# Kernel tuning notes

Measured on AMD Instinct MI355X. Metric: run time of the kernel, lower is better.

The kernel has to match this reference:

```python
import jax, jax.numpy as jnp
import numpy as np

N = 100000   # nodes
E = 1200000  # edges
D = 64       # feature / hidden dim (heads=1)
L = 3        # num_layers
G = 64       # num graphs
SCALE = 1.0 / np.sqrt(D)


def setup_inputs() -> dict:
    key = jax.random.key(0)
    ks = jax.random.split(key, 12)
    inp = {
        "x": jax.random.normal(ks[0], (N, D), dtype=jnp.float32),
        "edge_index": jax.random.randint(ks[1], (2, E), 0, N, dtype=jnp.int64),
        "batch": jnp.sort(jax.random.randint(ks[2], (N,), 0, G, dtype=jnp.int64)),
        "Wq": jax.random.normal(ks[3], (L, D, D), dtype=jnp.float32) * 0.1,
        "bq": jax.random.normal(ks[4], (L, D), dtype=jnp.float32) * 0.1,
        "Wk": jax.random.normal(ks[5], (L, D, D), dtype=jnp.float32) * 0.1,
        "bk": jax.random.normal(ks[6], (L, D), dtype=jnp.float32) * 0.1,
        "Wv": jax.random.normal(ks[7], (L, D, D), dtype=jnp.float32) * 0.1,
        "bv": jax.random.normal(ks[8], (L, D), dtype=jnp.float32) * 0.1,
        "Ws": jax.random.normal(ks[9], (L, D, D), dtype=jnp.float32) * 0.1,
        "bs": jax.random.normal(ks[10], (L, D), dtype=jnp.float32) * 0.1,
    }
    return inp


def _transformer_conv(x, src, dst, Wq, bq, Wk, bk, Wv, bv, Ws, bs):
    # PyG TransformerConv, heads=1, concat=True, root_weight=True, beta=False
    q = x @ Wq + bq            # [N, D] query of target nodes
    k = x @ Wk + bk            # [N, D] key of source nodes
    v = x @ Wv + bv            # [N, D] value of source nodes
    logits = jnp.sum(q[dst] * k[src], axis=-1) * SCALE  # [E]
    # segment softmax over incoming edges of each target node
    m = jax.ops.segment_max(logits, dst, num_segments=N)        # [N]
    e = jnp.exp(logits - m[dst])                                 # [E]
    denom = jax.ops.segment_sum(e, dst, num_segments=N)         # [N]
    alpha = e / denom[dst]                                       # [E]
    agg = jax.ops.segment_sum(alpha[:, None] * v[src], dst, num_segments=N)  # [N, D]
    return agg + x @ Ws + bs   # root/skip connection


def reference(x, edge_index, batch, Wq, bq, Wk, bk, Wv, bv, Ws, bs):
    src, dst = edge_index[0], edge_index[1]
    for l in range(L):
        x = _transformer_conv(x, src, dst, Wq[l], bq[l], Wk[l], bk[l],
                              Wv[l], bv[l], Ws[l], bs[l])
        x = jax.nn.relu(x)
    # global_mean_pool
    sums = jax.ops.segment_sum(x, batch, num_segments=G)                  # [G, D]
    counts = jax.ops.segment_sum(jnp.ones((N,), x.dtype), batch, num_segments=G)
    graph_emb = sums / jnp.maximum(counts, 1.0)[:, None]
    return (x, graph_emb)
```

## Files before the change

### kernel.cpp

```cpp
#include <hip/hip_runtime.h>
#include <math.h>

#define DD 64
#define APAD 512

typedef _Float16 h2 __attribute__((ext_vector_type(2)));
typedef _Float16 h4 __attribute__((ext_vector_type(4)));
typedef _Float16 h8 __attribute__((ext_vector_type(8)));
typedef float f32x4 __attribute__((ext_vector_type(4)));

__global__ __launch_bounds__(256) void k_prep(
    const float* __restrict__ Wq, const float* __restrict__ Wk,
    const float* __restrict__ Wv, const float* __restrict__ Ws,
    _Float16* __restrict__ wf,
    const float* __restrict__ x, _Float16* __restrict__ xb,
    int wblocks, int total8)
{
  int tid = threadIdx.x;
  if ((int)blockIdx.x < wblocks) {
    int id = blockIdx.x * 4 + (tid >> 6);
    int lane = tid & 63;
    int layer = id >> 5;
    int c = (id >> 1) & 15;
    int s = id & 1;
    int col = c * 16 + (lane & 15);
    int mi = col >> 6;
    const float* W = (mi == 0 ? Wq : mi == 1 ? Wk : mi == 2 ? Wv : Ws)
                     + (size_t)layer * DD * DD;
    int colw = col & 63;
    _Float16* o = wf + ((((size_t)(layer * 16 + c)) * 2 + s) * 64 + lane) * 8;
    #pragma unroll
    for (int j = 0; j < 8; ++j) {
      int k = s * 32 + (lane >> 4) * 8 + j;
      o[j] = (_Float16)W[k * DD + colw];
    }
  } else {
    int i = (blockIdx.x - wblocks) * 256 + tid;
    if (i >= total8) return;
    float4 a = ((const float4*)x)[i * 2];
    float4 b = ((const float4*)x)[i * 2 + 1];
    h8 o;
    o[0] = (_Float16)a.x; o[1] = (_Float16)a.y; o[2] = (_Float16)a.z; o[3] = (_Float16)a.w;
    o[4] = (_Float16)b.x; o[5] = (_Float16)b.y; o[6] = (_Float16)b.z; o[7] = (_Float16)b.w;
    *(h8*)(xb + (size_t)i * 8) = o;
  }
}

#define LH_STRIDE 200
#define LS_STRIDE 72
#define WAVE_LDS  (16 * 400 + 16 * 144)

__global__ __launch_bounds__(256) void k_projM(
    const _Float16* __restrict__ xb, const _Float16* __restrict__ wf,
    const float* __restrict__ bq, const float* __restrict__ bk,
    const float* __restrict__ bv, const float* __restrict__ bs,
    _Float16* __restrict__ qh, _Float16* __restrict__ kvh,
    _Float16* __restrict__ sh, int n)
{
  __shared__ __align__(16) char lds[4 * WAVE_LDS];
  int wave = threadIdx.x >> 6;
  int lane = threadIdx.x & 63;
  int nbase = blockIdx.x * 64 + wave * 16;
  if (nbase >= n) return;

  char* wbase = lds + wave * WAVE_LDS;
  _Float16* lh = (_Float16*)wbase;
  _Float16* ls = (_Float16*)(wbase + 16 * 400);

  const int cl = lane & 15;
  const int rq = lane >> 4;

  int ar = min(nbase + cl, n - 1);
  h8 a0 = *(const h8*)(xb + (size_t)ar * DD + rq * 8);
  h8 a1 = *(const h8*)(xb + (size_t)ar * DD + 32 + rq * 8);

  #pragma unroll
  for (int c = 0; c < 16; ++c) {
    const float* bp = (c < 4) ? bq : (c < 8) ? bk : (c < 12) ? bv : bs;
    const int fb = c * 16 + rq * 4;
    float4 b4 = *(const float4*)(bp + (fb & 63));
    f32x4 acc; acc[0] = b4.x; acc[1] = b4.y; acc[2] = b4.z; acc[3] = b4.w;
    const _Float16* wp = wf + ((size_t)(c * 2) * 64 + lane) * 8;
    h8 w0 = *(const h8*)(wp);
    h8 w1 = *(const h8*)(wp + 64 * 8);
    acc = __builtin_amdgcn_mfma_f32_16x16x32_f16(w0, a0, acc, 0, 0, 0);
    acc = __builtin_amdgcn_mfma_f32_16x16x32_f16(w1, a1, acc, 0, 0, 0);

    h4 o; o[0] = (_Float16)acc[0]; o[1] = (_Float16)acc[1];
    o[2] = (_Float16)acc[2]; o[3] = (_Float16)acc[3];
    if (c < 12)
      *(h4*)(lh + cl * LH_STRIDE + fb) = o;
    else
      *(h4*)(ls + cl * LS_STRIDE + (fb - 192)) = o;
  }

  #pragma unroll
  for (int i = 0; i < 2; ++i) {
    int chunk = i * 64 + lane;
    int nd = chunk >> 3, co = chunk & 7;
    h8 v = *(const h8*)(lh + nd * LH_STRIDE + co * 8);
    if (nbase + nd < n)
      *(h8*)(qh + (size_t)(nbase + nd) * DD + co * 8) = v;
  }
  #pragma unroll
  for (int i = 0; i < 4; ++i) {
    int chunk = i * 64 + lane;
    int nd = chunk >> 4, co = chunk & 15;
    h8 v = *(const h8*)(lh + nd * LH_STRIDE + 64 + co * 8);
    if (nbase + nd < n)
      *(h8*)(kvh + (size_t)(nbase + nd) * 128 + co * 8) = v;
  }
  #pragma unroll
  for (int i = 0; i < 2; ++i) {
    int chunk = i * 64 + lane;
    int nd = chunk >> 3, co = chunk & 7;
    h8 v = *(const h8*)(ls + nd * LS_STRIDE + co * 8);
    if (nbase + nd < n)
      *(h8*)(sh + (size_t)(nbase + nd) * DD + co * 8) = v;
  }
}

__global__ __launch_bounds__(256) void k_hist(
    const int* __restrict__ dst, int* __restrict__ deg,
    unsigned short* __restrict__ pos, int ecnt)
{
  int e = (blockIdx.x * 256 + threadIdx.x) * 4;
  if (e + 3 < ecnt) {
    int4 d = *(const int4*)(dst + e);
    pos[e]     = (unsigned short)atomicAdd(deg + d.x, 1);
    pos[e + 1] = (unsigned short)atomicAdd(deg + d.y, 1);
    pos[e + 2] = (unsigned short)atomicAdd(deg + d.z, 1);
    pos[e + 3] = (unsigned short)atomicAdd(deg + d.w, 1);
  } else {
    for (; e < ecnt; ++e)
      pos[e] = (unsigned short)atomicAdd(deg + dst[e], 1);
  }
}

__global__ __launch_bounds__(1024) void k_scanA(
    const int* __restrict__ deg, int* __restrict__ rowptr,
    int* __restrict__ btot, int* __restrict__ dbins, int n)
{
  __shared__ int wsum[16];
  __shared__ int lbin[256];
  int tid = threadIdx.x;
  int lane = tid & 63, wave = tid >> 6;
  if (tid < 256) lbin[tid] = 0;
  __syncthreads();
  int i = blockIdx.x * 4096 + tid * 4;
  int4 d = make_int4(0, 0, 0, 0);
  if (i + 3 < n) d = *(const int4*)(deg + i);
  else {
    if (i     < n) d.x = deg[i];
    if (i + 1 < n) d.y = deg[i + 1];
    if (i + 2 < n) d.z = deg[i + 2];
  }
  if (i     < n) atomicAdd(&lbin[min(d.x, 255)], 1);
  if (i + 1 < n) atomicAdd(&lbin[min(d.y, 255)], 1);
  if (i + 2 < n) atomicAdd(&lbin[min(d.z, 255)], 1);
  if (i + 3 < n) atomicAdd(&lbin[min(d.w, 255)], 1);

  int s1 = d.x, s2 = s1 + d.y, s3 = s2 + d.z, s4 = s3 + d.w;
  int s = s4;
  #pragma unroll
  for (int off = 1; off < 64; off <<= 1) {
    int t = __shfl_up(s, off);
    if (lane >= off) s += t;
  }
  if (lane == 63) wsum[wave] = s;
  __syncthreads();
  if (wave == 0) {
    int ws = (lane < 16) ? wsum[lane] : 0;
    #pragma unroll
    for (int off = 1; off < 16; off <<= 1) {
      int t = __shfl_up(ws, off);
      if (lane >= off) ws += t;
    }
    if (lane < 16) wsum[lane] = ws;
  }
  __syncthreads();
  int excl = ((wave > 0) ? wsum[wave - 1] : 0) + s - s4;
  if (i     < n) rowptr[i + 1] = excl + s1;
  if (i + 1 < n) rowptr[i + 2] = excl + s2;
  if (i + 2 < n) rowptr[i + 3] = excl + s3;
  if (i + 3 < n) rowptr[i + 4] = excl + s4;
  if (tid == 0) {
    if (blockIdx.x == 0) rowptr[0] = 0;
    btot[blockIdx.x] = wsum[15];
  }
  if (tid < 256 && lbin[tid]) atomicAdd(&dbins[tid], lbin[tid]);
}

__global__ __launch_bounds__(64) void k_scanB(
    int* __restrict__ btot, int nb, const int* __restrict__ dbins,
    int* __restrict__ dcur)
{
  int lane = threadIdx.x;
  int v = (lane < nb) ? btot[lane] : 0;
  int s = v;
  #pragma unroll
  for (int off = 1; off < 64; off <<= 1) {
    int t = __shfl_up(s, off);
    if (lane >= off) s += t;
  }
  if (lane < nb) btot[lane] = s - v;

  int4 dv = *(const int4*)(dbins + lane * 4);
  int t1 = dv.x, t2 = t1 + dv.y, t3 = t2 + dv.z, t4 = t3 + dv.w;
  int ss = t4;
  #pragma unroll
  for (int off = 1; off < 64; off <<= 1) {
    int t = __shfl_up(ss, off);
    if (lane >= off) ss += t;
  }
  int ex = ss - t4;
  dcur[lane * 4]     = ex;
  dcur[lane * 4 + 1] = ex + t1;
  dcur[lane * 4 + 2] = ex + t2;
  dcur[lane * 4 + 3] = ex + t3;
}

__global__ __launch_bounds__(1024) void k_scanCD(
    int* __restrict__ rowptr, const int* __restrict__ btot,
    const int* __restrict__ deg, int* __restrict__ dcur,
    int* __restrict__ order, int n, int nbk)
{
  __shared__ int lcnt[256];
  __shared__ int lbase[256];
  int tid = threadIdx.x;
  int b = blockIdx.x;
  if (b < nbk) {
    int off = btot[b];
    if (off) {
      int i = b * 4096 + tid * 4;
      #pragma unroll
      for (int k = 1; k <= 4; ++k)
        if (i + k <= n) rowptr[i + k] += off;
    }
  }
  if (tid < 256) lcnt[tid] = 0;
  __syncthreads();
  int i = b * 1024 + tid;
  int bin = 0, slot = 0;
  bool ok = (i < n);
  if (ok) {
    bin = min(deg[i], 255);
    slot = atomicAdd(&lcnt[bin], 1);
  }
  __syncthreads();
  if (tid < 256 && lcnt[tid]) lbase[tid] = atomicAdd(&dcur[tid], lcnt[tid]);
  __syncthreads();
  if (ok) order[(n - 1) - (lbase[bin] + slot)] = i;
}

__global__ __launch_bounds__(256) void k_fill(
    const int* __restrict__ src, const int* __restrict__ dst,
    const int* __restrict__ rowptr, const unsigned short* __restrict__ pos,
    int* __restrict__ adj, int ecnt)
{
  int e = (blockIdx.x * 256 + threadIdx.x) * 4;
  if (e + 3 < ecnt) {
    int4 d = *(const int4*)(dst + e);
    int4 s = *(const int4*)(src + e);
    ushort4 p = *(const ushort4*)(pos + e);
    adj[rowptr[d.x] + p.x] = s.x;
    adj[rowptr[d.y] + p.y] = s.y;
    adj[rowptr[d.z] + p.z] = s.z;
    adj[rowptr[d.w] + p.w] = s.w;
  } else {
    for (; e < ecnt; ++e)
      adj[rowptr[dst[e]] + pos[e]] = src[e];
  }
}

#define H2OF(v, i) __builtin_shufflevector((v), (v), 2*(i), 2*(i)+1)

template<bool LAST>
__global__ __launch_bounds__(256) void k_node(
    const _Float16* __restrict__ qh, const _Float16* __restrict__ kvh,
    const int* __restrict__ rowptr, const int* __restrict__ adj,
    const int* __restrict__ order,
    const _Float16* __restrict__ sh, float* __restrict__ outp,
    _Float16* __restrict__ xbnext, int n)
{
  int wid = (blockIdx.x * blockDim.x + threadIdx.x) >> 6;
  int lane = threadIdx.x & 63;
  const int g = lane >> 3;
  const int t = lane & 7;

  int idx = wid * 8 + g;
  bool nok = (idx < n);
  int node = order[nok ? idx : (n - 1)];

  const h8 q8 = *(const h8*)(qh + (size_t)node * DD + t * 8);
  const h2 qp0 = H2OF(q8, 0), qp1 = H2OF(q8, 1), qp2 = H2OF(q8, 2), qp3 = H2OF(q8, 3);

  const int e0 = rowptr[node];
  const int d  = nok ? (rowptr[node + 1] - e0) : 0;

  int dm = d;
  dm = max(dm, __shfl_xor(dm, 8));
  dm = max(dm, __shfl_xor(dm, 16));
  dm = max(dm, __shfl_xor(dm, 32));

  float mg = -1e30f, den = 0.f;
  float agg[8] = {0.f, 0.f, 0.f, 0.f, 0.f, 0.f, 0.f, 0.f};

  const char* kvb = (const char*)kvh;
  const unsigned tb = (unsigned)t << 4;

  h8 kP, vP;
  {
    int s = adj[e0];
    unsigned off = ((unsigned)s << 8) + tb;
    kP = *(const h8*)(kvb + off);
    vP = *(const h8*)(kvb + off + 128);
  }

  for (int it = 0; it < dm; ++it) {
    const h8 kc = kP, vc = vP;
    const bool valid = (it < d);
    {
      int s2 = adj[e0 + it + 1];
      unsigned off = ((unsigned)s2 << 8) + tb;
      kP = *(const h8*)(kvb + off);
      vP = *(const h8*)(kvb + off + 128);
    }

#if __has_builtin(__builtin_amdgcn_fdot2)
    float p = __builtin_amdgcn_fdot2(qp0, H2OF(kc, 0), 0.f, false);
    p = __builtin_amdgcn_fdot2(qp1, H2OF(kc, 1), p, false);
    p = __builtin_amdgcn_fdot2(qp2, H2OF(kc, 2), p, false);
    p = __builtin_amdgcn_fdot2(qp3, H2OF(kc, 3), p, false);
#else
    h2 ph = qp0 * H2OF(kc, 0);
    ph = qp1 * H2OF(kc, 1) + ph;
    ph = qp2 * H2OF(kc, 2) + ph;
    ph = qp3 * H2OF(kc, 3) + ph;
    float p = (float)ph.x + (float)ph.y;
#endif
    p += __shfl_xor(p, 1);
    p += __shfl_xor(p, 2);
    p += __shfl_xor(p, 4);
    p *= 0.125f;

    if (valid && p > mg) {
      float c = __expf(mg - p);
      den *= c;
      #pragma unroll
      for (int j = 0; j < 8; ++j) agg[j] *= c;
      mg = p;
    }
    float w = valid ? __expf(p - mg) : 0.f;
    den += w;
    #pragma unroll
    for (int j = 0; j < 8; ++j)
      agg[j] = fmaf(w, (float)vc[j], agg[j]);
  }

  if (nok) {
    float inv = (den > 0.f) ? (1.0f / den) : 0.f;
    const h8 s8 = *(const h8*)(sh + (size_t)node * DD + t * 8);
    float r[8];
    #pragma unroll
    for (int j = 0; j < 8; ++j)
      r[j] = fmaxf(fmaf(agg[j], inv, (float)s8[j]), 0.f);
    if (LAST) {
      float* op = outp + (size_t)node * DD + t * 8;
      *(float4*)(op)     = make_float4(r[0], r[1], r[2], r[3]);
      *(float4*)(op + 4) = make_float4(r[4], r[5], r[6], r[7]);
    } else {
      h8 xh;
      #pragma unroll
      for (int j = 0; j < 8; ++j) xh[j] = (_Float16)r[j];
      *(h8*)(xbnext + (size_t)node * DD + t * 8) = xh;
    }
  }
}

__global__ __launch_bounds__(64) void k_pool_sum(
    const float* __restrict__ x, const int* __restrict__ batch,
    float* __restrict__ gsum, int n)
{
  int lane = threadIdx.x;
  int n0 = blockIdx.x * 64;
  if (n0 >= n) return;
  int n1 = min(n0 + 64, n);
  float acc = 0.f;
  int g_prev = batch[n0];
  for (int nn = n0; nn < n1; ++nn) {
    int g = batch[nn];
    if (g != g_prev) {
      atomicAdd(gsum + (size_t)g_prev * DD + lane, acc);
      acc = 0.f; g_prev = g;
    }
    acc += x[(size_t)nn * DD + lane];
  }
  atomicAdd(gsum + (size_t)g_prev * DD + lane, acc);
}

__device__ __forceinline__ int lbound(const int* __restrict__ a, int n, int key)
{
  int lo = 0, hi = n;
  while (lo < hi) {
    int mid = (lo + hi) >> 1;
    if (a[mid] < key) lo = mid + 1; else hi = mid;
  }
  return lo;
}

__global__ __launch_bounds__(256) void k_pool_div(
    const float* __restrict__ gsum, const int* __restrict__ batch,
    float* __restrict__ emb, int gtot, int n)
{
  int gid = blockIdx.x * blockDim.x + threadIdx.x;
  if (gid >= gtot * DD) return;
  int g = gid >> 6;
  int cnt = lbound(batch, n, g + 1) - lbound(batch, n, g);
  emb[gid] = gsum[gid] / fmaxf((float)cnt, 1.0f);
}

extern "C" void kernel_launch(void* const* d_in, const int* in_sizes, int n_in,
                              void* d_out, int out_size, void* d_ws, size_t ws_size,
                              hipStream_t stream)
{
  const float* x_in  = (const float*)d_in[0];
  const int*   ei    = (const int*)  d_in[1];
  const int*   batch = (const int*)  d_in[2];
  const float* Wq = (const float*)d_in[3];
  const float* bq = (const float*)d_in[4];
  const float* Wk = (const float*)d_in[5];
  const float* bk = (const float*)d_in[6];
  const float* Wv = (const float*)d_in[7];
  const float* bv = (const float*)d_in[8];
  const float* Ws = (const float*)d_in[9];
  const float* bs = (const float*)d_in[10];

  const int nd     = in_sizes[0];
  const int n      = nd / DD;
  const int ecnt   = in_sizes[1] / 2;
  const int layers = in_sizes[3] / (DD * DD);
  const int gtot   = (out_size - nd) / DD;

  const int* src = ei;
  const int* dst = ei + ecnt;

  char* cur = (char*)d_ws;
  _Float16*  SH  = (_Float16*)cur;  cur += (size_t)nd * 2;
  _Float16*  XB  = (_Float16*)cur;  cur += (size_t)nd * 2;
  _Float16*  QH  = (_Float16*)cur;  cur += (size_t)nd * 2;
  _Float16*  KVH = (_Float16*)cur;  cur += (size_t)nd * 4;
  _Float16*  WF  = (_Float16*)cur;  cur += (size_t)layers * 16384 * 2;
  int* rowptr = (int*)cur;          cur += (size_t)(n + 4) * 4;
  int* adj    = (int*)cur;          cur += (size_t)(ecnt + APAD) * 4;
  int* deg    = (int*)cur;          cur += (size_t)n * 4;
  int* dbins  = (int*)cur;          cur += 256 * 4;
  int* dcur   = (int*)cur;          cur += 256 * 4;
  int* btot   = (int*)cur;          cur += 64 * 4;
  int* order  = (int*)cur;          cur += (size_t)n * 4;
  unsigned short* pos = (unsigned short*)cur; cur += (size_t)ecnt * 2;
  float* gsum = (float*)cur;        cur += (size_t)gtot * DD * 4;

  float* out = (float*)d_out;

  const int wblocks = layers * 8;
  const int xblocks = (n * 8 + 255) / 256;
  k_prep<<<wblocks + xblocks, 256, 0, stream>>>(Wq, Wk, Wv, Ws, WF,
                                                x_in, XB, wblocks, n * 8);
  hipMemsetAsync(adj + ecnt, 0, (size_t)(APAD + n + 256) * 4, stream);
  hipMemsetAsync(gsum, 0, (size_t)gtot * DD * 4, stream);
  const int eb4 = (ecnt + 1023) / 1024;
  k_hist<<<eb4, 256, 0, stream>>>(dst, deg, pos, ecnt);
  const int nbk = (n + 4095) / 4096;
  k_scanA<<<nbk, 1024, 0, stream>>>(deg, rowptr, btot, dbins, n);
  k_scanB<<<1, 64, 0, stream>>>(btot, nbk, dbins, dcur);
  const int dblk = (n + 1023) / 1024;
  k_scanCD<<<dblk, 1024, 0, stream>>>(rowptr, btot, deg, dcur, order, n, nbk);
  k_fill<<<eb4, 256, 0, stream>>>(src, dst, rowptr, pos, adj, ecnt);

  const int pj = (n + 63) / 64;
  const int nb = (n + 31) / 32;

  for (int l = 0; l < layers; ++l) {
    const size_t bo = (size_t)l * DD;
    k_projM<<<pj, 256, 0, stream>>>(XB, WF + (size_t)l * 16384,
                                    bq + bo, bk + bo, bv + bo, bs + bo,
                                    QH, KVH, SH, n);
    if (l == layers - 1)
      k_node<true><<<nb, 256, 0, stream>>>(QH, KVH, rowptr, adj, order,
                                           SH, out, XB, n);
    else
      k_node<false><<<nb, 256, 0, stream>>>(QH, KVH, rowptr, adj, order,
                                            SH, out, XB, n);
  }

  const int pbk = (n + 63) / 64;
  k_pool_sum<<<pbk, 64, 0, stream>>>(out, batch, gsum, n);
  const int fb = (gtot * DD + 255) / 256;
  k_pool_div<<<fb, 256, 0, stream>>>(gsum, batch, out + (size_t)nd, gtot, n);
}
```

Baseline: 334.0 us.

## Fuse histogram into prep kernel, merge memsets, add nontemporal hints in node kernel

Folds the degree-histogram kernel into the prep kernel as an extra block range and merges the two workspace memsets by relocating the graph-sum buffer. The node kernel loops only to each node's own degree instead of the wave-group max, removing the validity masking. Nontemporal load/store hints are applied to order, q, adjacency, skip and output accesses. These aim to cut launch overhead and cache pollution, at the cost of possible divergence and of hints that may hurt reused data.

Result: slower. 401.7 us (+20.3%).

```diff
diff --git a/kernel.cpp b/kernel.cpp
--- a/kernel.cpp
+++ b/kernel.cpp
@@ -14,11 +14,14 @@
     const float* __restrict__ Wv, const float* __restrict__ Ws,
     _Float16* __restrict__ wf,
     const float* __restrict__ x, _Float16* __restrict__ xb,
-    int wblocks, int total8)
+    const int* __restrict__ dst, int* __restrict__ deg,
+    unsigned short* __restrict__ pos,
+    int wb, int xb_, int total8, int ecnt)
 {
   int tid = threadIdx.x;
-  if ((int)blockIdx.x < wblocks) {
-    int id = blockIdx.x * 4 + (tid >> 6);
+  int bid = blockIdx.x;
+  if (bid < wb) {
+    int id = bid * 4 + (tid >> 6);
     int lane = tid & 63;
     int layer = id >> 5;
     int c = (id >> 1) & 15;
@@ -34,8 +37,8 @@
       int k = s * 32 + (lane >> 4) * 8 + j;
       o[j] = (_Float16)W[k * DD + colw];
     }
-  } else {
-    int i = (blockIdx.x - wblocks) * 256 + tid;
+  } else if (bid < wb + xb_) {
+    int i = (bid - wb) * 256 + tid;
     if (i >= total8) return;
     float4 a = ((const float4*)x)[i * 2];
     float4 b = ((const float4*)x)[i * 2 + 1];
@@ -43,6 +46,18 @@
     o[0] = (_Float16)a.x; o[1] = (_Float16)a.y; o[2] = (_Float16)a.z; o[3] = (_Float16)a.w;
     o[4] = (_Float16)b.x; o[5] = (_Float16)b.y; o[6] = (_Float16)b.z; o[7] = (_Float16)b.w;
     *(h8*)(xb + (size_t)i * 8) = o;
+  } else {
+    int e = ((bid - wb - xb_) * 256 + tid) * 4;
+    if (e + 3 < ecnt) {
+      int4 d = *(const int4*)(dst + e);
+      pos[e]     = (unsigned short)atomicAdd(deg + d.x, 1);
+      pos[e + 1] = (unsigned short)atomicAdd(deg + d.y, 1);
+      pos[e + 2] = (unsigned short)atomicAdd(deg + d.z, 1);
+      pos[e + 3] = (unsigned short)atomicAdd(deg + d.w, 1);
+    } else {
+      for (; e < ecnt; ++e)
+        pos[e] = (unsigned short)atomicAdd(deg + dst[e], 1);
+    }
   }
 }
 
@@ -117,23 +132,6 @@
     h8 v = *(const h8*)(ls + nd * LS_STRIDE + co * 8);
     if (nbase + nd < n)
       *(h8*)(sh + (size_t)(nbase + nd) * DD + co * 8) = v;
-  }
-}
-
-__global__ __launch_bounds__(256) void k_hist(
-    const int* __restrict__ dst, int* __restrict__ deg,
-    unsigned short* __restrict__ pos, int ecnt)
-{
-  int e = (blockIdx.x * 256 + threadIdx.x) * 4;
-  if (e + 3 < ecnt) {
-    int4 d = *(const int4*)(dst + e);
-    pos[e]     = (unsigned short)atomicAdd(deg + d.x, 1);
-    pos[e + 1] = (unsigned short)atomicAdd(deg + d.y, 1);
-    pos[e + 2] = (unsigned short)atomicAdd(deg + d.z, 1);
-    pos[e + 3] = (unsigned short)atomicAdd(deg + d.w, 1);
-  } else {
-    for (; e < ecnt; ++e)
-      pos[e] = (unsigned short)atomicAdd(deg + dst[e], 1);
   }
 }
 
@@ -290,19 +288,15 @@
 
   int idx = wid * 8 + g;
   bool nok = (idx < n);
-  int node = order[nok ? idx : (n - 1)];
-
-  const h8 q8 = *(const h8*)(qh + (size_t)node * DD + t * 8);
+  int node = __builtin_nontemporal_load(order + (nok ? idx : (n - 1)));
+
+  const h8 q8 = __builtin_nontemporal_load(
+      (const h8*)(qh + (size_t)node * DD + t * 8));
   const h2 qp0 = H2OF(q8, 0), qp1 = H2OF(q8, 1), qp2 = H2OF(q8, 2), qp3 = H2OF(q8, 3);
 
   const int e0 = rowptr[node];
   const int d  = nok ? (rowptr[node + 1] - e0) : 0;
 
-  int dm = d;
-  dm = max(dm, __shfl_xor(dm, 8));
-  dm = max(dm, __shfl_xor(dm, 16));
-  dm = max(dm, __shfl_xor(dm, 32));
-
   float mg = -1e30f, den = 0.f;
   float agg[8] = {0.f, 0.f, 0.f, 0.f, 0.f, 0.f, 0.f, 0.f};
 
@@ -311,17 +305,16 @@
 
   h8 kP, vP;
   {
-    int s = adj[e0];
+    int s = __builtin_nontemporal_load(adj + e0);
     unsigned off = ((unsigned)s << 8) + tb;
     kP = *(const h8*)(kvb + off);
     vP = *(const h8*)(kvb + off + 128);
   }
 
-  for (int it = 0; it < dm; ++it) {
+  for (int it = 0; it < d; ++it) {
     const h8 kc = kP, vc = vP;
-    const bool valid = (it < d);
     {
-      int s2 = adj[e0 + it + 1];
+      int s2 = __builtin_nontemporal_load(adj + e0 + it + 1);
       unsigned off = ((unsigned)s2 << 8) + tb;
       kP = *(const h8*)(kvb + off);
       vP = *(const h8*)(kvb + off + 128);
@@ -344,14 +337,14 @@
     p += __shfl_xor(p, 4);
     p *= 0.125f;
 
-    if (valid && p > mg) {
+    if (p > mg) {
       float c = __expf(mg - p);
       den *= c;
       #pragma unroll
       for (int j = 0; j < 8; ++j) agg[j] *= c;
       mg = p;
     }
-    float w = valid ? __expf(p - mg) : 0.f;
+    float w = __expf(p - mg);
     den += w;
     #pragma unroll
     for (int j = 0; j < 8; ++j)
@@ -360,20 +353,23 @@
 
   if (nok) {
     float inv = (den > 0.f) ? (1.0f / den) : 0.f;
-    const h8 s8 = *(const h8*)(sh + (size_t)node * DD + t * 8);
+    const h8 s8 = __builtin_nontemporal_load(
+        (const h8*)(sh + (size_t)node * DD + t * 8));
     float r[8];
     #pragma unroll
     for (int j = 0; j < 8; ++j)
       r[j] = fmaxf(fmaf(agg[j], inv, (float)s8[j]), 0.f);
     if (LAST) {
       float* op = outp + (size_t)node * DD + t * 8;
-      *(float4*)(op)     = make_float4(r[0], r[1], r[2], r[3]);
-      *(float4*)(op + 4) = make_float4(r[4], r[5], r[6], r[7]);
+      f32x4 ra; ra[0] = r[0]; ra[1] = r[1]; ra[2] = r[2]; ra[3] = r[3];
+      f32x4 rb; rb[0] = r[4]; rb[1] = r[5]; rb[2] = r[6]; rb[3] = r[7];
+      __builtin_nontemporal_store(ra, (f32x4*)(op));
+      __builtin_nontemporal_store(rb, (f32x4*)(op + 4));
     } else {
       h8 xh;
       #pragma unroll
       for (int j = 0; j < 8; ++j) xh[j] = (_Float16)r[j];
-      *(h8*)(xbnext + (size_t)node * DD + t * 8) = xh;
+      __builtin_nontemporal_store(xh, (h8*)(xbnext + (size_t)node * DD + t * 8));
     }
   }
 }
@@ -394,7 +390,7 @@
       atomicAdd(gsum + (size_t)g_prev * DD + lane, acc);
       acc = 0.f; g_prev = g;
     }
-    acc += x[(size_t)nn * DD + lane];
+    acc += __builtin_nontemporal_load(x + (size_t)nn * DD + lane);
   }
   atomicAdd(gsum + (size_t)g_prev * DD + lane, acc);
 }
@@ -455,28 +451,29 @@
   int* adj    = (int*)cur;          cur += (size_t)(ecnt + APAD) * 4;
   int* deg    = (int*)cur;          cur += (size_t)n * 4;
   int* dbins  = (int*)cur;          cur += 256 * 4;
+  float* gsum = (float*)cur;        cur += (size_t)gtot * DD * 4;
   int* dcur   = (int*)cur;          cur += 256 * 4;
   int* btot   = (int*)cur;          cur += 64 * 4;
   int* order  = (int*)cur;          cur += (size_t)n * 4;
   unsigned short* pos = (unsigned short*)cur; cur += (size_t)ecnt * 2;
-  float* gsum = (float*)cur;        cur += (size_t)gtot * DD * 4;
 
   float* out = (float*)d_out;
 
-  const int wblocks = layers * 8;
-  const int xblocks = (n * 8 + 255) / 256;
-  k_prep<<<wblocks + xblocks, 256, 0, stream>>>(Wq, Wk, Wv, Ws, WF,
-                                                x_in, XB, wblocks, n * 8);
-  hipMemsetAsync(adj + ecnt, 0, (size_t)(APAD + n + 256) * 4, stream);
-  hipMemsetAsync(gsum, 0, (size_t)gtot * DD * 4, stream);
-  const int eb4 = (ecnt + 1023) / 1024;
-  k_hist<<<eb4, 256, 0, stream>>>(dst, deg, pos, ecnt);
+  hipMemsetAsync(adj + ecnt, 0,
+                 (size_t)(APAD + n + 256 + gtot * DD) * 4, stream);
+
+  const int wb  = layers * 8;
+  const int xbk = (n * 8 + 255) / 256;
+  const int hbk = (ecnt + 1023) / 1024;
+  k_prep<<<wb + xbk + hbk, 256, 0, stream>>>(Wq, Wk, Wv, Ws, WF,
+                                             x_in, XB, dst, deg, pos,
+                                             wb, xbk, n * 8, ecnt);
   const int nbk = (n + 4095) / 4096;
   k_scanA<<<nbk, 1024, 0, stream>>>(deg, rowptr, btot, dbins, n);
   k_scanB<<<1, 64, 0, stream>>>(btot, nbk, dbins, dcur);
   const int dblk = (n + 1023) / 1024;
   k_scanCD<<<dblk, 1024, 0, stream>>>(rowptr, btot, deg, dcur, order, n, nbk);
-  k_fill<<<eb4, 256, 0, stream>>>(src, dst, rowptr, pos, adj, ecnt);
+  k_fill<<<hbk, 256, 0, stream>>>(src, dst, rowptr, pos, adj, ecnt);
 
   const int pj = (n + 63) / 64;
   const int nb = (n + 31) / 32;
```
